# Kernel tuning notes

Measured on AMD Instinct MI355X. Metric: run time of the kernel, lower is better.

The kernel has to match this reference:

```python
import jax, jax.numpy as jnp
import numpy as np

_MAX_SQRT_GRADIENT = 1000.0


@jax.custom_vjp
def sqrt_bound_derivative(x):
    return jnp.sqrt(x)

def _sbd_fwd(x):
    return jnp.sqrt(x), x

def _sbd_bwd(x, g):
    clipped_x4 = jnp.clip(4.0 * x, 1.0 / _MAX_SQRT_GRADIENT ** 2, None)
    return (g / jnp.sqrt(clipped_x4),)

sqrt_bound_derivative.defvjp(_sbd_fwd, _sbd_bwd)


def setup_inputs() -> dict:
    key = jax.random.key(0)
    ks = jax.random.split(key, 6)
    B, S, D, H = 4, 2048, 2560, 10
    bw = D // H  # 256
    activations = jax.random.normal(ks[0], (B, S, D), dtype=jnp.float32)
    position_ids = jnp.broadcast_to(jnp.arange(S, dtype=jnp.int64), (B, S))
    recurrent_param = jax.random.normal(ks[1], (D,), dtype=jnp.float32)
    input_gate_weight = jax.random.normal(ks[2], (H, bw, bw), dtype=jnp.float32) / np.sqrt(bw)
    input_gate_bias = jax.random.normal(ks[3], (H, bw), dtype=jnp.float32) * 0.1
    recurrent_gate_weight = jax.random.normal(ks[4], (H, bw, bw), dtype=jnp.float32) / np.sqrt(bw)
    recurrent_gate_bias = jax.random.normal(ks[5], (H, bw), dtype=jnp.float32) * 0.1
    return {
        "activations": activations,
        "position_ids": position_ids,
        "recurrent_param": recurrent_param,
        "input_gate_weight": input_gate_weight,
        "input_gate_bias": input_gate_bias,
        "recurrent_gate_weight": recurrent_gate_weight,
        "recurrent_gate_bias": recurrent_gate_bias,
    }


def _rglru(activations, position_ids, recurrent_param,
           input_gate_weight, input_gate_bias,
           recurrent_gate_weight, recurrent_gate_bias):
    B, S, D = activations.shape
    H, bw, _ = input_gate_weight.shape
    reset = (position_ids == 0)[:, :, None]  # [B, S, 1] bool

    x = activations.reshape(B, S, H, bw)
    # per-head gate projections (equivalent to torch baddbmm over heads)
    ig = jnp.einsum('bshi,hij->bshj', x, input_gate_weight) + input_gate_bias
    input_gate = jax.nn.sigmoid(ig.reshape(B, S, D))
    rg = jnp.einsum('bshi,hij->bshj', x, recurrent_gate_weight) + recurrent_gate_bias
    recurrent_gate = jax.nn.sigmoid(rg.reshape(B, S, D))

    log_a = -8.0 * recurrent_gate * jax.nn.softplus(recurrent_param)
    a = jnp.exp(log_a)                       # diagonal recurrence coeff
    a_square = jnp.exp(2.0 * log_a)

    gated_inputs = activations * input_gate
    multiplier = sqrt_bound_derivative(1.0 - a_square)
    multiplier = jnp.where(reset, 1.0, multiplier)
    normalized_x = gated_inputs * multiplier

    a = jnp.where(reset, 0.0, a)  # recurrent_gate * ~reset

    # linear scan over time in fp32 accumulation
    def step(h, inp):
        a_t, x_t = inp
        h = a_t * h + x_t
        return h, h

    h0 = jnp.zeros((B, D), dtype=jnp.float32)
    a_t = jnp.transpose(a, (1, 0, 2)).astype(jnp.float32)           # [S, B, D]
    x_t = jnp.transpose(normalized_x, (1, 0, 2)).astype(jnp.float32)
    _, ys = jax.lax.scan(step, h0, (a_t, x_t))
    return jnp.transpose(ys, (1, 0, 2)).astype(activations.dtype)


def reference(activations, position_ids, recurrent_param,
              input_gate_weight, input_gate_bias,
              recurrent_gate_weight, recurrent_gate_bias):
    return _rglru(activations, position_ids, recurrent_param,
                  input_gate_weight, input_gate_bias,
                  recurrent_gate_weight, recurrent_gate_bias)
```

## Files before the change

kernel.cpp:

```cpp
#include <hip/hip_runtime.h>
#include <hip/hip_bf16.h>

#define B_  4
#define S_  2048
#define D_  2560
#define H_  10
#define BW_ 256
#define NC_ 32
#define L_  64

typedef _Float16 f16;
typedef _Float16 f16x4 __attribute__((ext_vector_type(4)));
typedef _Float16 f16x8 __attribute__((ext_vector_type(8)));
typedef float    f32x4 __attribute__((ext_vector_type(4)));
typedef unsigned int uint32;

__global__ __launch_bounds__(256) void prep_kernel(
    const float* __restrict__ wig, const float* __restrict__ wrg,
    const float* __restrict__ rp,
    f16* __restrict__ wt_ig, f16* __restrict__ wt_rg, float* __restrict__ sp)
{
    int t = blockIdx.x * 256 + threadIdx.x;
    if (t < H_ * BW_ * BW_) {
        int h = t >> 16, rem = t & 65535;
        int j = rem >> 8, i = rem & 255;
        wt_ig[t] = (f16)wig[(h << 16) + (i << 8) + j];
        wt_rg[t] = (f16)wrg[(h << 16) + (i << 8) + j];
    }
    if (t < D_) {
        float x = rp[t];
        sp[t] = (x > 20.f) ? x : log1pf(__expf(x));
    }
}

__global__ __launch_bounds__(256, 1) void fused_kernel(
    const float* __restrict__ act,
    const f16* __restrict__ wt_ig, const f16* __restrict__ wt_rg,
    const float* __restrict__ big, const float* __restrict__ brg,
    const float* __restrict__ sp,
    uint32* __restrict__ packed, float* __restrict__ Hend,
    float* __restrict__ Pprod)
{
    const int g  = blockIdx.x;
    const int ch = blockIdx.y;
    const int h  = blockIdx.z;
    const int b = g >> 5, c = g & 31;
    const int r0 = (b << 11) + (c << 6);
    const int tid = threadIdx.x;
    const int lane = tid & 63;
    const int w = tid >> 6;
    const int gate = w & 1;
    const int n0 = ch * 128 + (w >> 1) * 64;
    const int l16 = lane & 15, lhi = lane >> 4;

    __shared__ f16 lds[64 * 256];

    {
        const float* abase = act + (size_t)r0 * D_ + (h << 8);
        #pragma unroll
        for (int i = 0; i < 16; i++) {
            int f = i * 256 + tid;
            int row = f >> 6;
            int k4 = (f & 63) << 2;
            float4 v = *(const float4*)(abase + (size_t)row * D_ + k4);
            f16x4 hv;
            hv[0] = (f16)v.x; hv[1] = (f16)v.y; hv[2] = (f16)v.z; hv[3] = (f16)v.w;
            *(f16x4*)&lds[row * 256 + (k4 ^ ((row & 7) << 3))] = hv;
        }
    }
    __syncthreads();

    const f16* wbase = (gate ? wt_rg : wt_ig) + (h << 16);
    f32x4 acc[4][4] = {};
    f16x8 ar[2][4], br[2][4];

    auto LDA = [&](int ks, f16x8* dst) {
        #pragma unroll
        for (int fm = 0; fm < 4; fm++) {
            int row = fm * 16 + l16;
            int k = ks * 32 + lhi * 8;
            dst[fm] = *(const f16x8*)&lds[row * 256 + (k ^ ((row & 7) << 3))];
        }
    };
    auto LDB = [&](int ks, f16x8* dst) {
        int ka = ks * 32 + lhi * 8;
        #pragma unroll
        for (int fn = 0; fn < 4; fn++) {
            int j = n0 + fn * 16 + l16;
            dst[fn] = *(const f16x8*)(wbase + (j << 8) + ka);
        }
    };

    LDA(0, ar[0]); LDB(0, br[0]);
    #pragma unroll
    for (int ks = 0; ks < 8; ks++) {
        const int cur = ks & 1;
        if (ks < 7) { LDA(ks + 1, ar[cur ^ 1]); LDB(ks + 1, br[cur ^ 1]); }
        #pragma unroll
        for (int fm = 0; fm < 4; fm++)
        #pragma unroll
        for (int fn = 0; fn < 4; fn++)
            acc[fm][fn] = __builtin_amdgcn_mfma_f32_16x16x32_f16(
                ar[cur][fm], br[cur][fn], acc[fm][fn], 0, 0, 0);
    }
    __syncthreads();

    {
        const float* biasp = gate ? brg : big;
        const int halfoff = gate ? 128 : 0;
        #pragma unroll
        for (int fn = 0; fn < 4; fn++) {
            int coll = (w >> 1) * 64 + fn * 16 + l16;
            int dcol = (h << 8) + ch * 128 + coll;
            float bias = biasp[dcol];
            float spv = sp[dcol];
            #pragma unroll
            for (int fm = 0; fm < 4; fm++)
            #pragma unroll
            for (int r = 0; r < 4; r++) {
                int rl = fm * 16 + lhi * 4 + r;
                float val = acc[fm][fn][r] + bias;
                float sig = 1.f / (1.f + __expf(-val));
                f16 ov = gate ? (f16)(-8.f * sig * spv) : (f16)sig;
                lds[rl * 256 + halfoff + (coll ^ ((rl & 7) << 3))] = ov;
            }
        }
    }
    __syncthreads();

    if (tid < 128) {
        const int t = tid;
        const bool chunk0 = (c == 0);
        const float* ap = act + (size_t)r0 * D_ + (h << 8) + ch * 128 + t;
        uint32* op = packed + (size_t)r0 * D_ + (h << 8) + ch * 128 + t;
        float hacc = 0.f, P = 1.f;
        #pragma unroll 4
        for (int s = 0; s < 64; s++) {
            int sw = t ^ ((s & 7) << 3);
            float ig = (float)lds[s * 256 + sw];
            float la = (float)lds[s * 256 + 128 + sw];
            float a = __expf(la);
            float x = ap[(size_t)s * D_] * ig;
            float mult;
            if (chunk0 && (s == 0)) { a = 0.f; mult = 1.f; }
            else mult = sqrtf(fmaxf(1.f - a * a, 0.f));
            hacc = fmaf(a, hacc, x * mult);
            P *= a;
            union { uint32 u; f16 hh[2]; } cv;
            cv.hh[0] = (f16)hacc; cv.hh[1] = (f16)P;
            op[(size_t)s * D_] = cv.u;
        }
        const int o = g * D_ + (h << 8) + ch * 128 + t;
        Hend[o]  = hacc;
        Pprod[o] = P;
    }
}

__global__ __launch_bounds__(256) void carry_kernel(
    const float* __restrict__ Hend, const float* __restrict__ Pprod,
    float* __restrict__ carry)
{
    const int d = blockIdx.x * 256 + threadIdx.x;
    const int b = blockIdx.y;
    float He[NC_], Pp[NC_];
    #pragma unroll
    for (int cc = 0; cc < NC_; cc++) {
        const int i = (b * NC_ + cc) * D_ + d;
        He[cc] = Hend[i];
        Pp[cc] = Pprod[i];
    }
    float cv = 0.f;
    #pragma unroll
    for (int cc = 0; cc < NC_; cc++) {
        carry[(b * NC_ + cc) * D_ + d] = cv;
        cv = fmaf(Pp[cc], cv, He[cc]);
    }
}

__global__ __launch_bounds__(256) void finalize_kernel(
    const uint32* __restrict__ packed, const float* __restrict__ carry,
    float* __restrict__ out)
{
    const uint32 n4 = (uint32)(B_ * S_ * D_) / 4;
    uint32 i4 = blockIdx.x * 256 + threadIdx.x;
    const uint32 stride = gridDim.x * 256;
    for (; i4 < n4; i4 += stride) {
        uint32 e = i4 * 4;
        uint32 grp = e / (L_ * D_);
        uint32 d = e % D_;
        uint4 p = ((const uint4*)packed)[i4];
        float4 cv = *(const float4*)(carry + grp * D_ + d);
        union { uint32 u; f16 hh[2]; } q;
        float4 o;
        q.u = p.x; o.x = fmaf((float)q.hh[1], cv.x, (float)q.hh[0]);
        q.u = p.y; o.y = fmaf((float)q.hh[1], cv.y, (float)q.hh[0]);
        q.u = p.z; o.z = fmaf((float)q.hh[1], cv.z, (float)q.hh[0]);
        q.u = p.w; o.w = fmaf((float)q.hh[1], cv.w, (float)q.hh[0]);
        ((float4*)out)[i4] = o;
    }
}

extern "C" void kernel_launch(void* const* d_in, const int* in_sizes, int n_in,
                              void* d_out, int out_size, void* d_ws, size_t ws_size,
                              hipStream_t stream)
{
    const float* act = (const float*)d_in[0];
    const float* rp  = (const float*)d_in[2];
    const float* wig = (const float*)d_in[3];
    const float* big = (const float*)d_in[4];
    const float* wrg = (const float*)d_in[5];
    const float* brg = (const float*)d_in[6];
    float* out = (float*)d_out;

    char* ws = (char*)d_ws;
    uint32* packed = (uint32*)ws;
    f16*   wt_ig = (f16*)(ws + (size_t)83886080);
    f16*   wt_rg = wt_ig + (size_t)H_ * BW_ * BW_;
    float* sp    = (float*)(wt_rg + (size_t)H_ * BW_ * BW_);
    float* Hend  = sp + D_;
    float* Pprod = Hend + (size_t)B_ * NC_ * D_;
    float* carry = Pprod + (size_t)B_ * NC_ * D_;

    hipLaunchKernelGGL(prep_kernel, dim3((H_ * BW_ * BW_ + 255) / 256), dim3(256),
                       0, stream, wig, wrg, rp, wt_ig, wt_rg, sp);
    hipLaunchKernelGGL(fused_kernel, dim3(B_ * NC_, 2, H_), dim3(256),
                       0, stream, act, wt_ig, wt_rg, big, brg, sp,
                       packed, Hend, Pprod);
    hipLaunchKernelGGL(carry_kernel, dim3(D_ / 256, B_), dim3(256),
                       0, stream, Hend, Pprod, carry);
    hipLaunchKernelGGL(finalize_kernel, dim3(2560), dim3(256),
                       0, stream, packed, carry, out);
}
```

Before: 268.8 us.

## Fuse carry propagation and finalize into scan kernel via ticketed decoupled lookback

Replaces the three-stage chunked scan (write packed f16 intermediates, carry kernel, finalize kernel) with a single kernel. Blocks take tickets in order, keep local scan results in LDS, publish chunk-end state with release flags, spin-wait on earlier chunks, compute their carry and write final outputs directly. This removes the large packed intermediate round-trip through global memory and two launches. Blocks now cover a full head (512 threads, two LDS buffers), and the weight transpose is tiled through LDS for coalesced access. The cost is serial spin-waiting, a per-block O(c) carry recompute, and a memset per call.

```diff
diff --git a/kernel.cpp b/kernel.cpp
--- a/kernel.cpp
+++ b/kernel.cpp
@@ -8,6 +8,8 @@
 #define BW_ 256
 #define NC_ 32
 #define L_  64
+#define NCHAIN (B_ * H_)
+#define NBLK (NCHAIN * NC_)
 
 typedef _Float16 f16;
 typedef _Float16 f16x4 __attribute__((ext_vector_type(4)));
@@ -20,52 +22,84 @@
     const float* __restrict__ rp,
     f16* __restrict__ wt_ig, f16* __restrict__ wt_rg, float* __restrict__ sp)
 {
-    int t = blockIdx.x * 256 + threadIdx.x;
-    if (t < H_ * BW_ * BW_) {
-        int h = t >> 16, rem = t & 65535;
-        int j = rem >> 8, i = rem & 255;
-        wt_ig[t] = (f16)wig[(h << 16) + (i << 8) + j];
-        wt_rg[t] = (f16)wrg[(h << 16) + (i << 8) + j];
-    }
-    if (t < D_) {
-        float x = rp[t];
-        sp[t] = (x > 20.f) ? x : log1pf(__expf(x));
+    __shared__ f16 tl[64 * 68];
+    const int it = blockIdx.x, jt = blockIdx.y, h = blockIdx.z;
+    const int tid = threadIdx.x;
+
+    int flat = ((blockIdx.z * 4 + blockIdx.y) * 4 + blockIdx.x) * 256 + tid;
+    if (flat < D_) {
+        float x = rp[flat];
+        sp[flat] = (x > 20.f) ? x : log1pf(__expf(x));
+    }
+
+    for (int m = 0; m < 2; m++) {
+        const float* W = m ? wrg : wig;
+        f16* WT = m ? wt_rg : wt_ig;
+        if (m) __syncthreads();
+        #pragma unroll
+        for (int p = 0; p < 4; p++) {
+            int idx = p * 256 + tid;
+            int il = idx >> 4, j4 = (idx & 15) << 2;
+            float4 v = *(const float4*)&W[(h << 16) + ((it * 64 + il) << 8)
+                                          + jt * 64 + j4];
+            f16x4 hv;
+            hv[0] = (f16)v.x; hv[1] = (f16)v.y; hv[2] = (f16)v.z; hv[3] = (f16)v.w;
+            *(f16x4*)&tl[il * 68 + j4] = hv;
+        }
+        __syncthreads();
+        #pragma unroll
+        for (int p = 0; p < 4; p++) {
+            int idx = p * 256 + tid;
+            int jl = idx >> 4, i4 = (idx & 15) << 2;
+            f16x4 hv;
+            hv[0] = tl[(i4 + 0) * 68 + jl];
+            hv[1] = tl[(i4 + 1) * 68 + jl];
+            hv[2] = tl[(i4 + 2) * 68 + jl];
+            hv[3] = tl[(i4 + 3) * 68 + jl];
+            *(f16x4*)&WT[(h << 16) + ((jt * 64 + jl) << 8) + it * 64 + i4] = hv;
+        }
     }
 }
 
-__global__ __launch_bounds__(256, 1) void fused_kernel(
+__global__ __launch_bounds__(512, 4) void fused_kernel(
     const float* __restrict__ act,
     const f16* __restrict__ wt_ig, const f16* __restrict__ wt_rg,
     const float* __restrict__ big, const float* __restrict__ brg,
     const float* __restrict__ sp,
-    uint32* __restrict__ packed, float* __restrict__ Hend,
-    float* __restrict__ Pprod)
+    float* __restrict__ He, float* __restrict__ Pp,
+    int* __restrict__ flags, int* __restrict__ counter,
+    float* __restrict__ out)
 {
-    const int g  = blockIdx.x;
-    const int ch = blockIdx.y;
-    const int h  = blockIdx.z;
-    const int b = g >> 5, c = g & 31;
+    __shared__ f16 lds1[64 * 256];
+    __shared__ f16 lds2[64 * 256];
+    __shared__ float carry_lds[256];
+    __shared__ int ticket_s;
+
+    const int tid = threadIdx.x;
+    if (tid == 0) ticket_s = atomicAdd(counter, 1);
+    __syncthreads();
+    const int t = ticket_s;
+    const int c = t & 31;
+    const int chain = t >> 5;
+    const int b = chain & 3, h = chain >> 2;
     const int r0 = (b << 11) + (c << 6);
-    const int tid = threadIdx.x;
-    const int lane = tid & 63;
-    const int w = tid >> 6;
+
+    const int lane = tid & 63, w = tid >> 6;
     const int gate = w & 1;
-    const int n0 = ch * 128 + (w >> 1) * 64;
+    const int n0 = (w >> 1) * 64;
     const int l16 = lane & 15, lhi = lane >> 4;
-
-    __shared__ f16 lds[64 * 256];
 
     {
         const float* abase = act + (size_t)r0 * D_ + (h << 8);
         #pragma unroll
-        for (int i = 0; i < 16; i++) {
-            int f = i * 256 + tid;
+        for (int i = 0; i < 8; i++) {
+            int f = i * 512 + tid;
             int row = f >> 6;
             int k4 = (f & 63) << 2;
             float4 v = *(const float4*)(abase + (size_t)row * D_ + k4);
             f16x4 hv;
             hv[0] = (f16)v.x; hv[1] = (f16)v.y; hv[2] = (f16)v.z; hv[3] = (f16)v.w;
-            *(f16x4*)&lds[row * 256 + (k4 ^ ((row & 7) << 3))] = hv;
+            *(f16x4*)&lds1[row * 256 + (k4 ^ ((row & 7) << 3))] = hv;
         }
     }
     __syncthreads();
@@ -79,7 +113,7 @@
         for (int fm = 0; fm < 4; fm++) {
             int row = fm * 16 + l16;
             int k = ks * 32 + lhi * 8;
-            dst[fm] = *(const f16x8*)&lds[row * 256 + (k ^ ((row & 7) << 3))];
+            dst[fm] = *(const f16x8*)&lds1[row * 256 + (k ^ ((row & 7) << 3))];
         }
     };
     auto LDB = [&](int ks, f16x8* dst) {
@@ -107,11 +141,11 @@
 
     {
         const float* biasp = gate ? brg : big;
-        const int halfoff = gate ? 128 : 0;
+        f16* ldst = gate ? lds2 : lds1;
         #pragma unroll
         for (int fn = 0; fn < 4; fn++) {
-            int coll = (w >> 1) * 64 + fn * 16 + l16;
-            int dcol = (h << 8) + ch * 128 + coll;
+            int coll = n0 + fn * 16 + l16;
+            int dcol = (h << 8) + coll;
             float bias = biasp[dcol];
             float spv = sp[dcol];
             #pragma unroll
@@ -122,81 +156,74 @@
                 float val = acc[fm][fn][r] + bias;
                 float sig = 1.f / (1.f + __expf(-val));
                 f16 ov = gate ? (f16)(-8.f * sig * spv) : (f16)sig;
-                lds[rl * 256 + halfoff + (coll ^ ((rl & 7) << 3))] = ov;
+                ldst[rl * 256 + (coll ^ ((rl & 7) << 3))] = ov;
             }
         }
     }
     __syncthreads();
 
-    if (tid < 128) {
-        const int t = tid;
+    if (tid < 256) {
         const bool chunk0 = (c == 0);
-        const float* ap = act + (size_t)r0 * D_ + (h << 8) + ch * 128 + t;
-        uint32* op = packed + (size_t)r0 * D_ + (h << 8) + ch * 128 + t;
+        const float* ap = act + (size_t)r0 * D_ + (h << 8) + tid;
         float hacc = 0.f, P = 1.f;
         #pragma unroll 4
         for (int s = 0; s < 64; s++) {
-            int sw = t ^ ((s & 7) << 3);
-            float ig = (float)lds[s * 256 + sw];
-            float la = (float)lds[s * 256 + 128 + sw];
+            int sw = tid ^ ((s & 7) << 3);
+            float ig = (float)lds1[s * 256 + sw];
+            float la = (float)lds2[s * 256 + sw];
             float a = __expf(la);
-            float x = ap[(size_t)s * D_] * ig;
+            float xv = ap[(size_t)s * D_];
             float mult;
             if (chunk0 && (s == 0)) { a = 0.f; mult = 1.f; }
             else mult = sqrtf(fmaxf(1.f - a * a, 0.f));
-            hacc = fmaf(a, hacc, x * mult);
+            hacc = fmaf(a, hacc, xv * ig * mult);
             P *= a;
-            union { uint32 u; f16 hh[2]; } cv;
-            cv.hh[0] = (f16)hacc; cv.hh[1] = (f16)P;
-            op[(size_t)s * D_] = cv.u;
-        }
-        const int o = g * D_ + (h << 8) + ch * 128 + t;
-        Hend[o]  = hacc;
-        Pprod[o] = P;
-    }
-}
-
-__global__ __launch_bounds__(256) void carry_kernel(
-    const float* __restrict__ Hend, const float* __restrict__ Pprod,
-    float* __restrict__ carry)
-{
-    const int d = blockIdx.x * 256 + threadIdx.x;
-    const int b = blockIdx.y;
-    float He[NC_], Pp[NC_];
-    #pragma unroll
-    for (int cc = 0; cc < NC_; cc++) {
-        const int i = (b * NC_ + cc) * D_ + d;
-        He[cc] = Hend[i];
-        Pp[cc] = Pprod[i];
-    }
-    float cv = 0.f;
-    #pragma unroll
-    for (int cc = 0; cc < NC_; cc++) {
-        carry[(b * NC_ + cc) * D_ + d] = cv;
-        cv = fmaf(Pp[cc], cv, He[cc]);
-    }
-}
-
-__global__ __launch_bounds__(256) void finalize_kernel(
-    const uint32* __restrict__ packed, const float* __restrict__ carry,
-    float* __restrict__ out)
-{
-    const uint32 n4 = (uint32)(B_ * S_ * D_) / 4;
-    uint32 i4 = blockIdx.x * 256 + threadIdx.x;
-    const uint32 stride = gridDim.x * 256;
-    for (; i4 < n4; i4 += stride) {
-        uint32 e = i4 * 4;
-        uint32 grp = e / (L_ * D_);
-        uint32 d = e % D_;
-        uint4 p = ((const uint4*)packed)[i4];
-        float4 cv = *(const float4*)(carry + grp * D_ + d);
-        union { uint32 u; f16 hh[2]; } q;
-        float4 o;
-        q.u = p.x; o.x = fmaf((float)q.hh[1], cv.x, (float)q.hh[0]);
-        q.u = p.y; o.y = fmaf((float)q.hh[1], cv.y, (float)q.hh[0]);
-        q.u = p.z; o.z = fmaf((float)q.hh[1], cv.z, (float)q.hh[0]);
-        q.u = p.w; o.w = fmaf((float)q.hh[1], cv.w, (float)q.hh[0]);
-        ((float4*)out)[i4] = o;
+            lds1[s * 256 + sw] = (f16)hacc;
+            lds2[s * 256 + sw] = (f16)P;
+        }
+        const size_t o = (size_t)(chain * NC_ + c) * 256 + tid;
+        He[o] = hacc;
+        Pp[o] = P;
+    }
+    __syncthreads();
+    if (tid == 0)
+        __hip_atomic_store(&flags[chain * NC_ + c], 1,
+                           __ATOMIC_RELEASE, __HIP_MEMORY_SCOPE_AGENT);
+
+    if (c > 0) {
+        if (tid < c) {
+            while (__hip_atomic_load(&flags[chain * NC_ + tid], __ATOMIC_RELAXED,
+                                     __HIP_MEMORY_SCOPE_AGENT) == 0)
+                __builtin_amdgcn_s_sleep(8);
+        }
+        __syncthreads();
+        __threadfence();
+        if (tid < 256) {
+            float cv = 0.f;
+            for (int j = 0; j < c; j++) {
+                const size_t o = (size_t)(chain * NC_ + j) * 256 + tid;
+                cv = fmaf(Pp[o], cv, He[o]);
+            }
+            carry_lds[tid] = cv;
+        }
+    } else {
+        if (tid < 256) carry_lds[tid] = 0.f;
+    }
+    __syncthreads();
+
+    {
+        const int col = tid & 255;
+        const int shalf = tid >> 8;
+        const float cva = carry_lds[col];
+        float* op = out + (size_t)(r0 + shalf * 32) * D_ + (h << 8) + col;
+        #pragma unroll 8
+        for (int si = 0; si < 32; si++) {
+            int s = shalf * 32 + si;
+            int sw = col ^ ((s & 7) << 3);
+            float ys = (float)lds1[s * 256 + sw];
+            float A  = (float)lds2[s * 256 + sw];
+            op[(size_t)si * D_] = fmaf(A, cva, ys);
+        }
     }
 }
 
@@ -213,21 +240,19 @@
     float* out = (float*)d_out;
 
     char* ws = (char*)d_ws;
-    uint32* packed = (uint32*)ws;
-    f16*   wt_ig = (f16*)(ws + (size_t)83886080);
+    f16*   wt_ig = (f16*)ws;
     f16*   wt_rg = wt_ig + (size_t)H_ * BW_ * BW_;
     float* sp    = (float*)(wt_rg + (size_t)H_ * BW_ * BW_);
-    float* Hend  = sp + D_;
-    float* Pprod = Hend + (size_t)B_ * NC_ * D_;
-    float* carry = Pprod + (size_t)B_ * NC_ * D_;
-
-    hipLaunchKernelGGL(prep_kernel, dim3((H_ * BW_ * BW_ + 255) / 256), dim3(256),
+    float* He    = sp + D_;
+    float* Pp    = He + (size_t)NBLK * 256;
+    int*   flags = (int*)(Pp + (size_t)NBLK * 256);
+    int*   counter = flags + NBLK;
+
+    hipMemsetAsync(flags, 0, (NBLK + 1) * sizeof(int), stream);
+
+    hipLaunchKernelGGL(prep_kernel, dim3(4, 4, H_), dim3(256),
                        0, stream, wig, wrg, rp, wt_ig, wt_rg, sp);
-    hipLaunchKernelGGL(fused_kernel, dim3(B_ * NC_, 2, H_), dim3(256),
+    hipLaunchKernelGGL(fused_kernel, dim3(NBLK), dim3(512),
                        0, stream, act, wt_ig, wt_rg, big, brg, sp,
-                       packed, Hend, Pprod);
-    hipLaunchKernelGGL(carry_kernel, dim3(D_ / 256, B_), dim3(256),
-                       0, stream, Hend, Pprod, carry);
-    hipLaunchKernelGGL(finalize_kernel, dim3(2560), dim3(256),
-                       0, stream, packed, carry, out);
+                       He, Pp, flags, counter, out);
 }
```

Result: slower. 572.8 us (+113.1%).
